# Kernel tuning notes

Measured on AMD Instinct MI355X. Metric: run time of the kernel, lower is better.

## Reference

```python
import jax, jax.numpy as jnp
import numpy as np

B, NV, C = 2, 25000, 32
NR, ND, F = 3, 16, 64


def setup_inputs() -> dict:
    key = jax.random.key(0)
    k1, k2, k3, k4 = jax.random.split(key, 4)
    y = jax.random.normal(k1, (B, NV, C), dtype=jnp.float32)
    # exp_map[..., 0] = batch index, exp_map[..., 1] = vertex index (geodesic patch)
    vert = jax.random.randint(k2, (B, NV, NR, ND), 0, NV, dtype=jnp.int32)
    batch_idx = jnp.broadcast_to(jnp.arange(B, dtype=jnp.int32)[:, None, None, None], (B, NV, NR, ND))
    exp_map = jnp.stack([batch_idx, vert], axis=-1)  # (B, NV, NR, ND, 2)
    kernel = jax.random.normal(k3, (NR, ND, C, F), dtype=jnp.float32) * 0.05
    center_kernel = jax.random.normal(k4, (C, F), dtype=jnp.float32) * 0.05
    bias = jnp.zeros((F,), dtype=jnp.float32)
    return {"y": y, "exp_map": exp_map, "kernel": kernel,
            "center_kernel": center_kernel, "bias": bias}


def reference(y, exp_map, kernel, center_kernel, bias):
    b, nv, c = y.shape
    nr, nd, _, f = kernel.shape
    # gather_nd: per-vertex geodesic patches -> (B, NV, NR, ND, C)
    patches = y[exp_map[..., 0], exp_map[..., 1]]
    p = patches.reshape(b * nv, nr, nd, c)
    # cyclic pad along direction axis: width 2*ND-1 so VALID conv yields ND outputs
    p = jnp.concatenate([p, p[:, :, :-1, :]], axis=2)  # (B*NV, NR, 2*ND-1, C)
    z = jax.lax.conv_general_dilated(
        p, kernel, window_strides=(1, 1), padding='VALID',
        dimension_numbers=('NHWC', 'HWIO', 'NHWC'))  # (B*NV, 1, ND, F)
    z = z.reshape(b, nv, nd, f)
    # center vertex term, broadcast over directions
    z = z + (y @ center_kernel)[:, :, None, :]
    z = z + bias
    z = jax.nn.relu(z)
    # take_max over orientations
    return jnp.max(z, axis=2)  # (B, NV, F)
```

## Files before the change

kernel.cpp:

```cpp
#include <hip/hip_runtime.h>
#include <stdint.h>

#define NVERT 25000
#define NPAIR 25000
#define NGRP  12500

typedef __bf16  bf16x8 __attribute__((ext_vector_type(8)));
typedef float   f32x16 __attribute__((ext_vector_type(16)));

#define NCHUNK 98
#define BPACK_HALF_USHORT (NCHUNK*512)
#define LDS_B   (NCHUNK*1024)
#define ROWB    80
#define VSTRIDE (49*ROWB)
#define WSTRIDE (4*VSTRIDE)
#define LDS_TOT (LDS_B + 4*WSTRIDE)

__device__ __forceinline__ unsigned short f2bf(float f) {
  unsigned int u = __float_as_uint(f);
  u += 0x7FFFu + ((u >> 16) & 1u);
  return (unsigned short)(u >> 16);
}

__device__ __forceinline__ uint2 pack4(float4 v) {
  uint2 r;
  r.x = (unsigned)f2bf(v.x) | ((unsigned)f2bf(v.y) << 16);
  r.y = (unsigned)f2bf(v.z) | ((unsigned)f2bf(v.w) << 16);
  return r;
}

__device__ __forceinline__ bf16x8 rot16(bf16x8 x) {
  union { bf16x8 v; int i[4]; } u;
  u.v = x;
#pragma unroll
  for (int k = 0; k < 4; ++k)
    u.i[k] = __builtin_amdgcn_update_dpp(0, u.i[k], 0x12F, 0xF, 0xF, true);
  return u.v;
}

__global__ __launch_bounds__(256) void prepack_kernel(
    const float* __restrict__ kern, const float* __restrict__ ckern,
    unsigned short* __restrict__ bpack)
{
  int tid = blockIdx.x*256 + threadIdx.x;
  if (tid >= 2*BPACK_HALF_USHORT) return;
  int fh  = tid / BPACK_HALF_USHORT;
  int rem = tid - fh*BPACK_HALF_USHORT;
  int kc  = rem >> 9;
  int e   = rem & 511;
  int l   = e >> 3, i = e & 7;
  int f   = fh*32 + (l & 31);
  int kk  = ((l >> 5) << 3) + i;
  float v;
  if (kc < 96) {
    int r = kc >> 5, ch = (kc >> 4) & 1, j = kc & 15;
    int c = ch*16 + kk;
    v = kern[((r*16 + j)*32 + c)*64 + f];
  } else {
    int c = (kc - 96)*16 + kk;
    v = ckern[c*64 + f];
  }
  bpack[tid] = f2bf(v);
}

#define CHUNK_GROUP(rr, cc)                                                    \
  {                                                                            \
    const char* ap = pbase + q*VSTRIDE + ((rr)*16 + d)*ROWB + (cc)*32 + hi*16; \
    bf16x8 a0 = *(const bf16x8*)ap;                                            \
    bf16x8 a1 = *(const bf16x8*)(ap + 2*VSTRIDE);                              \
    const char* bp = bbase + (size_t)(((rr)*2 + (cc))*16) * 1024;              \
    bf16x8 b0 = *(const bf16x8*)bp;                                            \
    bf16x8 b1 = *(const bf16x8*)(bp + 1024);                                   \
    _Pragma("unroll")                                                          \
    for (int j = 0; j < 16; ++j) {                                             \
      const bf16x8 b = b0;                                                     \
      b0 = b1;                                                                 \
      if (j < 14) b1 = *(const bf16x8*)(bp + (size_t)(j+2)*1024);              \
      acc0 = __builtin_amdgcn_mfma_f32_32x32x16_bf16(a0, b, acc0, 0, 0, 0);    \
      acc1 = __builtin_amdgcn_mfma_f32_32x32x16_bf16(a1, b, acc1, 0, 0, 0);    \
      if (j < 15) { a0 = rot16(a0); a1 = rot16(a1); }                          \
    }                                                                          \
  }

__global__ __launch_bounds__(256, 1) void conv_kernel(
    const float* __restrict__ y,
    const int*   __restrict__ em,
    const float* __restrict__ bias,
    const unsigned short* __restrict__ bpack,
    float* __restrict__ out)
{
  extern __shared__ __align__(16) char smem[];
  const int fh  = blockIdx.x & 1;
  const int bl  = blockIdx.x >> 1;
  const int tid = threadIdx.x;
  const int w   = tid >> 6;
  const int l   = tid & 63;

  {
    const uint4* src = (const uint4*)(bpack + (size_t)fh * BPACK_HALF_USHORT);
    uint4* dst = (uint4*)smem;
    for (int idx = tid; idx < LDS_B/16; idx += 256) dst[idx] = src[idx];
  }
  __syncthreads();

  char* pbase = smem + LDS_B + w * WSTRIDE;
  const char* bbase = smem + (size_t)l * 16;
  const float biasv = bias[fh*32 + (l & 31)];
  const int gw = bl*4 + w;
  const int q  = (l >> 4) & 1;
  const int d  = l & 15;
  const int hi = l >> 5;
  const int2* em2 = (const int2*)em;
  const int rsl = l >> 3, cp = l & 7;

  int g = gw;
  bool valid = (g < NGRP);

  if (valid) {
    int2 e0[24];
#pragma unroll
    for (int it = 0; it < 24; ++it)
      e0[it] = em2[(g*4 + (it & 3))*48 + (it >> 2)*8 + rsl];
    float4 yv0[25];
#pragma unroll
    for (int it = 0; it < 24; ++it)
      yv0[it] = *(const float4*)(y + ((size_t)e0[it].x*NVERT + (size_t)e0[it].y)*32 + cp*4);
    yv0[24] = *(const float4*)(y + (size_t)(g*4 + (rsl & 3))*32 + cp*4);
#pragma unroll
    for (int it = 0; it < 24; ++it)
      *(uint2*)(pbase + (it & 3)*VSTRIDE + ((it >> 2)*8 + rsl)*ROWB + cp*8) = pack4(yv0[it]);
    if (l < 32)
      *(uint2*)(pbase + rsl*VSTRIDE + 48*ROWB + cp*8) = pack4(yv0[24]);
  }

  for (int t = 0; t < 25; ++t) {
    if (!valid) break;
    const int gn = g + 512;
    const bool vnext = (gn < NGRP);

    int2 e[24];
    if (vnext) {
#pragma unroll
      for (int it = 0; it < 24; ++it)
        e[it] = em2[(gn*4 + (it & 3))*48 + (it >> 2)*8 + rsl];
    }

    f32x16 acc0, acc1;
#pragma unroll
    for (int k = 0; k < 16; ++k) { acc0[k] = 0.f; acc1[k] = 0.f; }

    CHUNK_GROUP(0, 0)
    CHUNK_GROUP(0, 1)

    float4 yv[25];
    if (vnext) {
#pragma unroll
      for (int it = 0; it < 24; ++it)
        yv[it] = *(const float4*)(y + ((size_t)e[it].x*NVERT + (size_t)e[it].y)*32 + cp*4);
      yv[24] = *(const float4*)(y + (size_t)(gn*4 + (rsl & 3))*32 + cp*4);
    }

    CHUNK_GROUP(1, 0)
    CHUNK_GROUP(1, 1)
    CHUNK_GROUP(2, 0)
    CHUNK_GROUP(2, 1)
#pragma unroll
    for (int ch = 0; ch < 2; ++ch) {
      const bf16x8 b = *(const bf16x8*)(bbase + (size_t)(96 + ch)*1024);
      const char* ap = pbase + q*VSTRIDE + 48*ROWB + ch*32 + hi*16;
      bf16x8 a0 = *(const bf16x8*)ap;
      bf16x8 a1 = *(const bf16x8*)(ap + 2*VSTRIDE);
      acc0 = __builtin_amdgcn_mfma_f32_32x32x16_bf16(a0, b, acc0, 0, 0, 0);
      acc1 = __builtin_amdgcn_mfma_f32_32x32x16_bf16(a1, b, acc1, 0, 0, 0);
    }

    {
      float m0 = acc0[0], m1 = acc0[8];
#pragma unroll
      for (int k = 1; k < 8; ++k) { m0 = fmaxf(m0, acc0[k]); m1 = fmaxf(m1, acc0[8+k]); }
      m0 = fmaxf(m0, __shfl_xor(m0, 32, 64));
      m1 = fmaxf(m1, __shfl_xor(m1, 32, 64));
      float v = (hi ? m1 : m0) + biasv;
      out[(size_t)(g*4 + hi)*64 + fh*32 + (l & 31)] = fmaxf(v, 0.f);
    }
    {
      float m0 = acc1[0], m1 = acc1[8];
#pragma unroll
      for (int k = 1; k < 8; ++k) { m0 = fmaxf(m0, acc1[k]); m1 = fmaxf(m1, acc1[8+k]); }
      m0 = fmaxf(m0, __shfl_xor(m0, 32, 64));
      m1 = fmaxf(m1, __shfl_xor(m1, 32, 64));
      float v = (hi ? m1 : m0) + biasv;
      out[(size_t)(g*4 + 2 + hi)*64 + fh*32 + (l & 31)] = fmaxf(v, 0.f);
    }

    if (vnext) {
#pragma unroll
      for (int it = 0; it < 24; ++it)
        *(uint2*)(pbase + (it & 3)*VSTRIDE + ((it >> 2)*8 + rsl)*ROWB + cp*8) = pack4(yv[it]);
      if (l < 32)
        *(uint2*)(pbase + rsl*VSTRIDE + 48*ROWB + cp*8) = pack4(yv[24]);
    }

    g = gn; valid = vnext;
  }
}

extern "C" void kernel_launch(void* const* d_in, const int* in_sizes, int n_in,
                              void* d_out, int out_size, void* d_ws, size_t ws_size,
                              hipStream_t stream) {
  const float* y     = (const float*)d_in[0];
  const int*   em    = (const int*)  d_in[1];
  const float* kern  = (const float*)d_in[2];
  const float* ckern = (const float*)d_in[3];
  const float* bias  = (const float*)d_in[4];
  float* out = (float*)d_out;
  unsigned short* bpack = (unsigned short*)d_ws;

  hipFuncSetAttribute(reinterpret_cast<const void*>(conv_kernel),
                      hipFuncAttributeMaxDynamicSharedMemorySize, LDS_TOT);

  prepack_kernel<<<(2*BPACK_HALF_USHORT + 255)/256, 256, 0, stream>>>(kern, ckern, bpack);
  conv_kernel<<<256, 256, LDS_TOT, stream>>>(y, em, bias, bpack, out);
}
```

Before: 239.3 us.

## Split channel reduction across paired waves with 512-thread blocks and LDS partial-sum merge

```diff
diff --git a/kernel.cpp b/kernel.cpp
--- a/kernel.cpp
+++ b/kernel.cpp
@@ -1,4 +1,5 @@
 #include <hip/hip_runtime.h>
+#include <hip/hip_bf16.h>
 #include <stdint.h>
 
 #define NVERT 25000
@@ -16,17 +17,23 @@
 #define WSTRIDE (4*VSTRIDE)
 #define LDS_TOT (LDS_B + 4*WSTRIDE)
 
+__device__ __forceinline__ uint2 pack4(float4 v) {
+  union { __hip_bfloat162 h; unsigned u; } a, b;
+  a.h = __float22bfloat162_rn(float2{v.x, v.y});
+  b.h = __float22bfloat162_rn(float2{v.z, v.w});
+  return uint2{a.u, b.u};
+}
+
+__device__ __forceinline__ unsigned pk2(float a, float b) {
+  union { __hip_bfloat162 h; unsigned u; } t;
+  t.h = __float22bfloat162_rn(float2{a, b});
+  return t.u;
+}
+
 __device__ __forceinline__ unsigned short f2bf(float f) {
   unsigned int u = __float_as_uint(f);
   u += 0x7FFFu + ((u >> 16) & 1u);
   return (unsigned short)(u >> 16);
-}
-
-__device__ __forceinline__ uint2 pack4(float4 v) {
-  uint2 r;
-  r.x = (unsigned)f2bf(v.x) | ((unsigned)f2bf(v.y) << 16);
-  r.y = (unsigned)f2bf(v.z) | ((unsigned)f2bf(v.w) << 16);
-  return r;
 }
 
 __device__ __forceinline__ bf16x8 rot16(bf16x8 x) {
@@ -63,12 +70,12 @@
   bpack[tid] = f2bf(v);
 }
 
-#define CHUNK_GROUP(rr, cc)                                                    \
+#define PASS(rr)                                                               \
   {                                                                            \
-    const char* ap = pbase + q*VSTRIDE + ((rr)*16 + d)*ROWB + (cc)*32 + hi*16; \
+    const char* ap = pbase + q*VSTRIDE + ((rr)*16 + d)*ROWB + choff + hi*16;   \
     bf16x8 a0 = *(const bf16x8*)ap;                                            \
     bf16x8 a1 = *(const bf16x8*)(ap + 2*VSTRIDE);                              \
-    const char* bp = bbase + (size_t)(((rr)*2 + (cc))*16) * 1024;              \
+    const char* bp = bbase + (size_t)(((rr)*2 + ch)*16) * 1024;                \
     bf16x8 b0 = *(const bf16x8*)bp;                                            \
     bf16x8 b1 = *(const bf16x8*)(bp + 1024);                                   \
     _Pragma("unroll")                                                          \
@@ -82,7 +89,7 @@
     }                                                                          \
   }
 
-__global__ __launch_bounds__(256, 1) void conv_kernel(
+__global__ __launch_bounds__(512, 2) void conv_kernel(
     const float* __restrict__ y,
     const int*   __restrict__ em,
     const float* __restrict__ bias,
@@ -94,22 +101,25 @@
   const int bl  = blockIdx.x >> 1;
   const int tid = threadIdx.x;
   const int w   = tid >> 6;
+  const int tm  = w & 3;
+  const int ch  = w >> 2;
   const int l   = tid & 63;
 
   {
     const uint4* src = (const uint4*)(bpack + (size_t)fh * BPACK_HALF_USHORT);
     uint4* dst = (uint4*)smem;
-    for (int idx = tid; idx < LDS_B/16; idx += 256) dst[idx] = src[idx];
-  }
-  __syncthreads();
-
-  char* pbase = smem + LDS_B + w * WSTRIDE;
+    for (int idx = tid; idx < LDS_B/16; idx += 512) dst[idx] = src[idx];
+  }
+
+  char* pbase = smem + LDS_B + tm * WSTRIDE;
   const char* bbase = smem + (size_t)l * 16;
   const float biasv = bias[fh*32 + (l & 31)];
-  const int gw = bl*4 + w;
+  const int gw = bl*4 + tm;
   const int q  = (l >> 4) & 1;
   const int d  = l & 15;
   const int hi = l >> 5;
+  const int choff = ch*32;
+  const int chv = ch*2;
   const int2* em2 = (const int2*)em;
   const int rsl = l >> 3, cp = l & 7;
 
@@ -117,88 +127,124 @@
   bool valid = (g < NGRP);
 
   if (valid) {
-    int2 e0[24];
-#pragma unroll
-    for (int it = 0; it < 24; ++it)
-      e0[it] = em2[(g*4 + (it & 3))*48 + (it >> 2)*8 + rsl];
-    float4 yv0[25];
-#pragma unroll
-    for (int it = 0; it < 24; ++it)
+    int2 e0[12];
+#pragma unroll
+    for (int it = 0; it < 12; ++it)
+      e0[it] = em2[(g*4 + chv + (it & 1))*48 + (it >> 1)*8 + rsl];
+    float4 yv0[12];
+#pragma unroll
+    for (int it = 0; it < 12; ++it)
       yv0[it] = *(const float4*)(y + ((size_t)e0[it].x*NVERT + (size_t)e0[it].y)*32 + cp*4);
-    yv0[24] = *(const float4*)(y + (size_t)(g*4 + (rsl & 3))*32 + cp*4);
-#pragma unroll
-    for (int it = 0; it < 24; ++it)
-      *(uint2*)(pbase + (it & 3)*VSTRIDE + ((it >> 2)*8 + rsl)*ROWB + cp*8) = pack4(yv0[it]);
-    if (l < 32)
-      *(uint2*)(pbase + rsl*VSTRIDE + 48*ROWB + cp*8) = pack4(yv0[24]);
+    float4 yc0;
+    if (l < 16) yc0 = *(const float4*)(y + (size_t)(g*4 + chv + rsl)*32 + cp*4);
+#pragma unroll
+    for (int it = 0; it < 12; ++it)
+      *(uint2*)(pbase + (chv + (it & 1))*VSTRIDE + ((it >> 1)*8 + rsl)*ROWB + cp*8) = pack4(yv0[it]);
+    if (l < 16)
+      *(uint2*)(pbase + (chv + rsl)*VSTRIDE + 48*ROWB + cp*8) = pack4(yc0);
   }
 
   for (int t = 0; t < 25; ++t) {
     if (!valid) break;
+    __syncthreads();
+
     const int gn = g + 512;
     const bool vnext = (gn < NGRP);
 
-    int2 e[24];
+    int2 e[12];
     if (vnext) {
 #pragma unroll
-      for (int it = 0; it < 24; ++it)
-        e[it] = em2[(gn*4 + (it & 3))*48 + (it >> 2)*8 + rsl];
+      for (int it = 0; it < 12; ++it)
+        e[it] = em2[(gn*4 + chv + (it & 1))*48 + (it >> 1)*8 + rsl];
     }
 
     f32x16 acc0, acc1;
 #pragma unroll
     for (int k = 0; k < 16; ++k) { acc0[k] = 0.f; acc1[k] = 0.f; }
 
-    CHUNK_GROUP(0, 0)
-    CHUNK_GROUP(0, 1)
-
-    float4 yv[25];
+    PASS(0)
+
+    float4 yv[12], yc;
     if (vnext) {
 #pragma unroll
-      for (int it = 0; it < 24; ++it)
+      for (int it = 0; it < 12; ++it)
         yv[it] = *(const float4*)(y + ((size_t)e[it].x*NVERT + (size_t)e[it].y)*32 + cp*4);
-      yv[24] = *(const float4*)(y + (size_t)(gn*4 + (rsl & 3))*32 + cp*4);
-    }
-
-    CHUNK_GROUP(1, 0)
-    CHUNK_GROUP(1, 1)
-    CHUNK_GROUP(2, 0)
-    CHUNK_GROUP(2, 1)
-#pragma unroll
-    for (int ch = 0; ch < 2; ++ch) {
-      const bf16x8 b = *(const bf16x8*)(bbase + (size_t)(96 + ch)*1024);
-      const char* ap = pbase + q*VSTRIDE + 48*ROWB + ch*32 + hi*16;
-      bf16x8 a0 = *(const bf16x8*)ap;
-      bf16x8 a1 = *(const bf16x8*)(ap + 2*VSTRIDE);
-      acc0 = __builtin_amdgcn_mfma_f32_32x32x16_bf16(a0, b, acc0, 0, 0, 0);
-      acc1 = __builtin_amdgcn_mfma_f32_32x32x16_bf16(a1, b, acc1, 0, 0, 0);
-    }
-
+      if (l < 16) yc = *(const float4*)(y + (size_t)(gn*4 + chv + rsl)*32 + cp*4);
+    }
+
+    PASS(1)
+    PASS(2)
     {
-      float m0 = acc0[0], m1 = acc0[8];
-#pragma unroll
-      for (int k = 1; k < 8; ++k) { m0 = fmaxf(m0, acc0[k]); m1 = fmaxf(m1, acc0[8+k]); }
-      m0 = fmaxf(m0, __shfl_xor(m0, 32, 64));
-      m1 = fmaxf(m1, __shfl_xor(m1, 32, 64));
-      float v = (hi ? m1 : m0) + biasv;
-      out[(size_t)(g*4 + hi)*64 + fh*32 + (l & 31)] = fmaxf(v, 0.f);
-    }
-    {
-      float m0 = acc1[0], m1 = acc1[8];
-#pragma unroll
-      for (int k = 1; k < 8; ++k) { m0 = fmaxf(m0, acc1[k]); m1 = fmaxf(m1, acc1[8+k]); }
-      m0 = fmaxf(m0, __shfl_xor(m0, 32, 64));
-      m1 = fmaxf(m1, __shfl_xor(m1, 32, 64));
-      float v = (hi ? m1 : m0) + biasv;
-      out[(size_t)(g*4 + 2 + hi)*64 + fh*32 + (l & 31)] = fmaxf(v, 0.f);
+      const bf16x8 bc = *(const bf16x8*)(bbase + (size_t)(96 + ch)*1024);
+      const char* c0 = pbase + q*VSTRIDE + 48*ROWB + choff + hi*16;
+      bf16x8 a0 = *(const bf16x8*)c0;
+      bf16x8 a1 = *(const bf16x8*)(c0 + 2*VSTRIDE);
+      acc0 = __builtin_amdgcn_mfma_f32_32x32x16_bf16(a0, bc, acc0, 0, 0, 0);
+      acc1 = __builtin_amdgcn_mfma_f32_32x32x16_bf16(a1, bc, acc1, 0, 0, 0);
+    }
+
+    __syncthreads();
+
+    if (ch) {
+      uint4 s0 = {pk2(acc0[0],acc0[1]),  pk2(acc0[2],acc0[3]),
+                  pk2(acc0[4],acc0[5]),  pk2(acc0[6],acc0[7])};
+      uint4 s1 = {pk2(acc0[8],acc0[9]),  pk2(acc0[10],acc0[11]),
+                  pk2(acc0[12],acc0[13]),pk2(acc0[14],acc0[15])};
+      uint4 s2 = {pk2(acc1[0],acc1[1]),  pk2(acc1[2],acc1[3]),
+                  pk2(acc1[4],acc1[5]),  pk2(acc1[6],acc1[7])};
+      uint4 s3 = {pk2(acc1[8],acc1[9]),  pk2(acc1[10],acc1[11]),
+                  pk2(acc1[12],acc1[13]),pk2(acc1[14],acc1[15])};
+      *(uint4*)(pbase + 0*1024 + l*16) = s0;
+      *(uint4*)(pbase + 1*1024 + l*16) = s1;
+      *(uint4*)(pbase + 2*1024 + l*16) = s2;
+      *(uint4*)(pbase + 3*1024 + l*16) = s3;
+    }
+
+    __syncthreads();
+
+    if (!ch) {
+      uint4 x0 = *(const uint4*)(pbase + 0*1024 + l*16);
+      uint4 x1 = *(const uint4*)(pbase + 1*1024 + l*16);
+      uint4 x2 = *(const uint4*)(pbase + 2*1024 + l*16);
+      uint4 x3 = *(const uint4*)(pbase + 3*1024 + l*16);
+#pragma unroll
+      for (int k = 0; k < 4; ++k) {
+        unsigned u0 = (&x0.x)[k], u1 = (&x1.x)[k], u2 = (&x2.x)[k], u3 = (&x3.x)[k];
+        acc0[2*k]   += __uint_as_float(u0 << 16);
+        acc0[2*k+1] += __uint_as_float(u0 & 0xffff0000u);
+        acc0[8+2*k]   += __uint_as_float(u1 << 16);
+        acc0[8+2*k+1] += __uint_as_float(u1 & 0xffff0000u);
+        acc1[2*k]   += __uint_as_float(u2 << 16);
+        acc1[2*k+1] += __uint_as_float(u2 & 0xffff0000u);
+        acc1[8+2*k]   += __uint_as_float(u3 << 16);
+        acc1[8+2*k+1] += __uint_as_float(u3 & 0xffff0000u);
+      }
+      {
+        float m0 = acc0[0], m1 = acc0[8];
+#pragma unroll
+        for (int k = 1; k < 8; ++k) { m0 = fmaxf(m0, acc0[k]); m1 = fmaxf(m1, acc0[8+k]); }
+        m0 = fmaxf(m0, __shfl_xor(m0, 32, 64));
+        m1 = fmaxf(m1, __shfl_xor(m1, 32, 64));
+        float v = (hi ? m1 : m0) + biasv;
+        out[(size_t)(g*4 + hi)*64 + fh*32 + (l & 31)] = fmaxf(v, 0.f);
+      }
+      {
+        float m0 = acc1[0], m1 = acc1[8];
+#pragma unroll
+        for (int k = 1; k < 8; ++k) { m0 = fmaxf(m0, acc1[k]); m1 = fmaxf(m1, acc1[8+k]); }
+        m0 = fmaxf(m0, __shfl_xor(m0, 32, 64));
+        m1 = fmaxf(m1, __shfl_xor(m1, 32, 64));
+        float v = (hi ? m1 : m0) + biasv;
+        out[(size_t)(g*4 + 2 + hi)*64 + fh*32 + (l & 31)] = fmaxf(v, 0.f);
+      }
     }
 
     if (vnext) {
 #pragma unroll
-      for (int it = 0; it < 24; ++it)
-        *(uint2*)(pbase + (it & 3)*VSTRIDE + ((it >> 2)*8 + rsl)*ROWB + cp*8) = pack4(yv[it]);
-      if (l < 32)
-        *(uint2*)(pbase + rsl*VSTRIDE + 48*ROWB + cp*8) = pack4(yv[24]);
+      for (int it = 0; it < 12; ++it)
+        *(uint2*)(pbase + (chv + (it & 1))*VSTRIDE + ((it >> 1)*8 + rsl)*ROWB + cp*8) = pack4(yv[it]);
+      if (l < 16)
+        *(uint2*)(pbase + (chv + rsl)*VSTRIDE + 48*ROWB + cp*8) = pack4(yc);
     }
 
     g = gn; valid = vnext;
@@ -220,5 +266,5 @@
                       hipFuncAttributeMaxDynamicSharedMemorySize, LDS_TOT);
 
   prepack_kernel<<<(2*BPACK_HALF_USHORT + 255)/256, 256, 0, stream>>>(kern, ckern, bpack);
-  conv_kernel<<<256, 256, LDS_TOT, stream>>>(y, em, bias, bpack, out);
-}
+  conv_kernel<<<256, 512, LDS_TOT, stream>>>(y, em, bias, bpack, out);
+}
```

After: 222.8 us. 1.07x faster.
